# Performance work log

Measured on AMD Instinct MI355X. Metric: run time of the kernel, lower is better.

## Reference

```python
import jax, jax.numpy as jnp
import numpy as np

NBINS = 256       # kornia equalize_clahe default histogram bins
GRID = (8, 8)     # kornia default grid_size


def _clahe(x, clip_limit):
    """kornia-style CLAHE on x:(C,H,W) in [0,1]; H,W divisible by GRID."""
    C, H, W = x.shape
    GH, GW = GRID
    TH, TW = H // GH, W // GW
    pixels = TH * TW
    # ---- per-tile histograms via flat scatter-add (irregular core) ----
    b_hist = jnp.clip((x * NBINS).astype(jnp.int32), 0, NBINS - 1)  # torch.histc(min=0,max=1) bins
    tiles = b_hist.reshape(C, GH, TH, GW, TW).transpose(0, 1, 3, 2, 4).reshape(-1, pixels)
    ntiles = tiles.shape[0]  # C*GH*GW
    flat = (tiles + (jnp.arange(ntiles, dtype=jnp.int32) * NBINS)[:, None]).ravel()
    hist = jnp.zeros((ntiles * NBINS,), x.dtype).at[flat].add(1.0).reshape(ntiles, NBINS)
    # ---- clip and redistribute excess (kornia _compute_luts) ----
    max_val = jnp.maximum(jnp.floor(clip_limit * pixels / NBINS), 1.0)
    clipped = jnp.minimum(hist, max_val)
    excess = pixels - clipped.sum(-1)                    # (ntiles,), >= 0
    residual = jnp.mod(excess, NBINS)
    redist = (excess - residual) / NBINS
    hist = clipped + redist[:, None] + (jnp.arange(NBINS) < residual[:, None]).astype(x.dtype)
    # ---- LUT from CDF ----
    lut = jnp.floor(jnp.clip(jnp.cumsum(hist, -1) * (NBINS - 1) / pixels, 0, NBINS - 1))
    lut = lut.reshape(C, GH, GW, NBINS)
    # ---- per-pixel bilinear interpolation between 4 neighbouring tile LUTs ----
    def coords(n, T, G):
        g = (jnp.arange(n) + 0.5) / T - 0.5    # fractional tile coordinate
        lo = jnp.clip(jnp.floor(g), 0, G - 1).astype(jnp.int32)
        hi = jnp.clip(lo + 1, 0, G - 1)
        w = jnp.clip(g - jnp.floor(g), 0.0, 1.0).astype(x.dtype)
        return lo, hi, w
    y0, y1, wy = coords(H, TH, GH)
    x0, x1, wx = coords(W, TW, GW)
    b = jnp.clip(jnp.floor(x * (NBINS - 1)).astype(jnp.int32), 0, NBINS - 1)  # lookup bin
    c = jnp.arange(C)[:, None, None]
    def g(ty, tx):  # gather lut[c, ty[h], tx[w], b[c,h,w]] -> (C,H,W)
        return lut[c, ty[None, :, None], tx[None, None, :], b]
    top = g(y0, x0) * (1 - wx)[None, None, :] + g(y0, x1) * wx[None, None, :]
    bot = g(y1, x0) * (1 - wx)[None, None, :] + g(y1, x1) * wx[None, None, :]
    out = top * (1 - wy)[None, :, None] + bot * wy[None, :, None]
    return out / (NBINS - 1)


def _forward(x, log_cor=True):
    shape = x.shape
    mean = x.mean()
    std = jnp.std(x, ddof=1)            # torch .std() is unbiased
    x = (x - mean) / std                # TF.normalize
    xmin, xmax = x.min(), x.max()
    x = (x - xmin) / (xmax - xmin)      # normalize_in_range(x, 0, 1)
    ct_proxy = jnp.std(x, ddof=1)       # x.std([0,1,2]) on 3D input = scalar
    def clahe_branch(xx):
        beta = 10.0 * ct_proxy
        cl = 1.0 / (1.0 - beta) + beta  # data-dependent clip limit
        return _clahe(xx, cl)
    x = jax.lax.cond(ct_proxy < 0.05, clahe_branch, lambda xx: xx, x)
    if log_cor:
        x = jnp.log2(1.0 + x)           # adjust_log with gain=1
    return x.reshape(shape)


def setup_inputs() -> dict:
    key = jax.random.key(0)
    x = jax.random.normal(key, (32, 1024, 1024), dtype=jnp.float32)
    # heavy-tailed distribution -> std/range (ct_proxy) ~ 0.01 < 0.05 so CLAHE branch runs
    x = x ** 3
    return {"x": x}


def reference(x):
    return _forward(x, log_cor=True)
```

## Files before the change

### kernel.cpp

```cpp
#include <hip/hip_runtime.h>
#include <math.h>

#define NC 32
#define NH 1024
#define NW 1024
#define NTH 128
#define NTW 128
#define NBINS 256
#define NTILES (NC*8*8)
#define NPIXTOT (NC*NH*NW)
#define TPIX (NTH*NTW)

#define OFF_PSUM   0
#define OFF_PSQ    16384
#define OFF_PMIN   32768
#define OFF_PMAX   40960
#define OFF_PARAMS 49152
#define OFF_LUT8   65536

__global__ __launch_bounds__(256) void k_reduce(const float* __restrict__ x,
                                                double* __restrict__ ps,
                                                double* __restrict__ ps2,
                                                float* __restrict__ pmn,
                                                float* __restrict__ pmx) {
    int tid = threadIdx.x;
    long g = (long)blockIdx.x * 256 + tid;
    double s = 0.0, s2 = 0.0;
    float mn = INFINITY, mx = -INFINITY;
    const float4* x4 = (const float4*)x;
    const long n4 = NPIXTOT / 4;
    for (long i = g; i < n4; i += (long)2048 * 256) {
        float4 v = x4[i];
        float sf  = (v.x + v.y) + (v.z + v.w);
        float s2f = fmaf(v.x, v.x, fmaf(v.y, v.y, fmaf(v.z, v.z, v.w * v.w)));
        s  += (double)sf;
        s2 += (double)s2f;
        mn = fminf(mn, fminf(fminf(v.x, v.y), fminf(v.z, v.w)));
        mx = fmaxf(mx, fmaxf(fmaxf(v.x, v.y), fmaxf(v.z, v.w)));
    }
    for (int o = 32; o; o >>= 1) {
        s  += __shfl_down(s, o);
        s2 += __shfl_down(s2, o);
        mn = fminf(mn, __shfl_down(mn, o));
        mx = fmaxf(mx, __shfl_down(mx, o));
    }
    __shared__ double shs[4], shs2[4];
    __shared__ float shmn[4], shmx[4];
    int wid = tid >> 6, lane = tid & 63;
    if (lane == 0) { shs[wid] = s; shs2[wid] = s2; shmn[wid] = mn; shmx[wid] = mx; }
    __syncthreads();
    if (tid == 0) {
        double S  = shs[0] + shs[1] + shs[2] + shs[3];
        double S2 = shs2[0] + shs2[1] + shs2[2] + shs2[3];
        float MN = fminf(fminf(shmn[0], shmn[1]), fminf(shmn[2], shmn[3]));
        float MX = fmaxf(fmaxf(shmx[0], shmx[1]), fmaxf(shmx[2], shmx[3]));
        ps[blockIdx.x] = S; ps2[blockIdx.x] = S2; pmn[blockIdx.x] = MN; pmx[blockIdx.x] = MX;
    }
}

__global__ __launch_bounds__(256) void k_params(const double* __restrict__ ps,
                                                const double* __restrict__ ps2,
                                                const float* __restrict__ pmn,
                                                const float* __restrict__ pmx,
                                                float* __restrict__ params) {
    int tid = threadIdx.x;
    double s = 0.0, s2 = 0.0;
    float mn = INFINITY, mx = -INFINITY;
    for (int i = tid; i < 2048; i += 256) {
        s += ps[i]; s2 += ps2[i];
        mn = fminf(mn, pmn[i]); mx = fmaxf(mx, pmx[i]);
    }
    for (int o = 32; o; o >>= 1) {
        s  += __shfl_down(s, o);
        s2 += __shfl_down(s2, o);
        mn = fminf(mn, __shfl_down(mn, o));
        mx = fmaxf(mx, __shfl_down(mx, o));
    }
    __shared__ double shs[4], shs2[4];
    __shared__ float shmn[4], shmx[4];
    int wid = tid >> 6, lane = tid & 63;
    if (lane == 0) { shs[wid] = s; shs2[wid] = s2; shmn[wid] = mn; shmx[wid] = mx; }
    __syncthreads();
    if (tid == 0) {
        double S  = shs[0] + shs[1] + shs[2] + shs[3];
        double S2 = shs2[0] + shs2[1] + shs2[2] + shs2[3];
        float MN = fminf(fminf(shmn[0], shmn[1]), fminf(shmn[2], shmn[3]));
        float MX = fmaxf(fmaxf(shmx[0], shmx[1]), fmaxf(shmx[2], shmx[3]));
        const double n = (double)NPIXTOT;
        double var = (S2 - S * S / n) / (n - 1.0);
        double sd = sqrt(var > 0.0 ? var : 0.0);
        double range = (double)MX - (double)MN;
        double ct = sd / range;
        int flag = (ct < 0.05) ? 1 : 0;
        double beta = 10.0 * ct;
        double cl = 1.0 / (1.0 - beta) + beta;
        double mv = floor(cl * (double)TPIX / (double)NBINS);
        if (mv < 1.0) mv = 1.0;
        params[0] = MN;
        params[1] = (float)(1.0 / range);
        params[2] = (float)mv;
        ((int*)params)[3] = flag;
    }
}

__global__ __launch_bounds__(256) void k_histlut(const float* __restrict__ x,
                                                 const float* __restrict__ params,
                                                 unsigned char* __restrict__ lut8) {
    __shared__ unsigned lh[4 * NBINS];
    __shared__ int sh[NBINS];
    int tid = threadIdx.x;
    int t = blockIdx.x;
    int lane = tid & 63;
    int wid = tid >> 6;
    #pragma unroll
    for (int w = 0; w < 4; w++) lh[w * NBINS + tid] = 0;
    __syncthreads();
    float xmin = params[0], inv = params[1];
    int c = t >> 6, gy = (t >> 3) & 7, gx = t & 7;
    const float* base = x + ((long)c * NH + (long)gy * NTH) * NW + gx * NTW;
    unsigned* mylh = lh + wid * NBINS;
    #pragma unroll 4
    for (int j = 0; j < 16; j++) {
        int l = j * 256 + tid;
        int th = l >> 5, tw4 = l & 31;
        float4 v = *(const float4*)(base + (long)th * NW + tw4 * 4);
        float zv[4] = {v.x, v.y, v.z, v.w};
        #pragma unroll
        for (int k = 0; k < 4; k++) {
            float z = (zv[k] - xmin) * inv;
            int b = (int)(z * 256.0f);
            b = b < 0 ? 0 : (b > 255 ? 255 : b);
            unsigned long long alive = __ballot(1);
            #pragma unroll
            for (int r = 0; r < 3; r++) {
                if (!alive) break;
                int leader = (int)(__ffsll((long long)alive) - 1);
                int lb = __shfl(b, leader);
                unsigned long long m = __ballot(b == lb) & alive;
                if (lane == leader) atomicAdd(&mylh[lb], (unsigned)__popcll(m));
                alive &= ~m;
            }
            if ((alive >> lane) & 1ull) atomicAdd(&mylh[b], 1u);
        }
    }
    __syncthreads();
    int mv = (int)params[2];
    int h = (int)(lh[tid] + lh[NBINS + tid] + lh[2 * NBINS + tid] + lh[3 * NBINS + tid]);
    int cl = h < mv ? h : mv;
    sh[tid] = cl;
    __syncthreads();
    for (int o = 1; o < NBINS; o <<= 1) {
        int v = (tid >= o) ? sh[tid - o] : 0;
        __syncthreads();
        sh[tid] += v;
        __syncthreads();
    }
    int total = sh[NBINS - 1];
    int cdfc = sh[tid];
    int excess = TPIX - total;
    int residual = excess & (NBINS - 1);
    int redist = excess >> 8;
    int cdf = cdfc + redist * (tid + 1) + ((tid + 1) < residual ? (tid + 1) : residual);
    float lv = floorf(fminf((float)cdf * 255.0f / 16384.0f, 255.0f));
    int iv = (int)(lv < 0.0f ? 0.0f : lv);
    lut8[t * NBINS + tid] = (unsigned char)iv;
}

__global__ __launch_bounds__(256) void k_out(const float* __restrict__ x,
                                             const float* __restrict__ params,
                                             const unsigned char* __restrict__ lut8,
                                             float* __restrict__ out) {
    __shared__ unsigned char slut[4096];
    int tid = threadIdx.x;
    int r = blockIdx.x;
    int c = r >> 10;
    int h = r & (NH - 1);
    float xmin = params[0], inv = params[1];
    int flag = ((const int*)params)[3];
    float gy = (h + 0.5f) * (1.0f / NTH) - 0.5f;
    float fy = floorf(gy);
    float wy = gy - fy;
    int y0 = (int)fy; y0 = y0 < 0 ? 0 : (y0 > 7 ? 7 : y0);
    int y1 = y0 + 1 > 7 ? 7 : y0 + 1;
    const unsigned char* src0 = lut8 + ((long)c * 64 + y0 * 8) * NBINS;
    const unsigned char* src1 = lut8 + ((long)c * 64 + y1 * 8) * NBINS;
    if (tid < 128) {
        *(uint4*)(slut + tid * 16) = *(const uint4*)(src0 + tid * 16);
    } else {
        int u = tid - 128;
        *(uint4*)(slut + 2048 + u * 16) = *(const uint4*)(src1 + u * 16);
    }
    __syncthreads();
    long p = ((long)r << 10) + tid * 4;
    float4 v = *(const float4*)(x + p);
    float zv[4] = {v.x, v.y, v.z, v.w};
    float o4[4];
    #pragma unroll
    for (int k = 0; k < 4; k++) {
        float z = (zv[k] - xmin) * inv;
        float val;
        if (flag) {
            int wk = tid * 4 + k;
            float gxc = (wk + 0.5f) * (1.0f / NTW) - 0.5f;
            float fx = floorf(gxc);
            float wx = gxc - fx;
            int x0 = (int)fx; x0 = x0 < 0 ? 0 : (x0 > 7 ? 7 : x0);
            int x1 = x0 + 1 > 7 ? 7 : x0 + 1;
            int b = (int)(z * 255.0f);
            b = b < 0 ? 0 : (b > 255 ? 255 : b);
            float l00 = (float)slut[x0 * NBINS + b];
            float l01 = (float)slut[x1 * NBINS + b];
            float l10 = (float)slut[2048 + x0 * NBINS + b];
            float l11 = (float)slut[2048 + x1 * NBINS + b];
            float top = l00 * (1.0f - wx) + l01 * wx;
            float bot = l10 * (1.0f - wx) + l11 * wx;
            val = (top * (1.0f - wy) + bot * wy) * (1.0f / 255.0f);
        } else {
            val = z;
        }
        o4[k] = log2f(1.0f + val);
    }
    *(float4*)(out + p) = make_float4(o4[0], o4[1], o4[2], o4[3]);
}

extern "C" void kernel_launch(void* const* d_in, const int* in_sizes, int n_in,
                              void* d_out, int out_size, void* d_ws, size_t ws_size,
                              hipStream_t stream) {
    const float* x = (const float*)d_in[0];
    float* out = (float*)d_out;
    char* ws = (char*)d_ws;
    double* ps   = (double*)(ws + OFF_PSUM);
    double* ps2  = (double*)(ws + OFF_PSQ);
    float* pmn   = (float*)(ws + OFF_PMIN);
    float* pmx   = (float*)(ws + OFF_PMAX);
    float* params= (float*)(ws + OFF_PARAMS);
    unsigned char* lut8 = (unsigned char*)(ws + OFF_LUT8);

    k_reduce<<<2048, 256, 0, stream>>>(x, ps, ps2, pmn, pmx);
    k_params<<<1, 256, 0, stream>>>(ps, ps2, pmn, pmx, params);
    k_histlut<<<NTILES, 256, 0, stream>>>(x, params, lut8);
    k_out<<<NC * NH, 256, 0, stream>>>(x, params, lut8, out);
}
```

Baseline: 297.8 us.

## Fuse param reduction into histogram kernel and simplify wave-aggregated binning

Removes the single-block k_params launch: every histogram block now redundantly reduces the 2048 partials itself, and block 0 writes params for the output kernel. The histogram inner loop replaces the ballot/leader peeling loop with a single wave-uniform dominant bin taken from lane 0's first pixel. All four pixels per lane are compared against it and counted with one xor-shuffle reduction, and non-matching pixels fall back to per-pixel LDS atomics. The reduction kernel also unrolls by two with split double accumulators to add memory-level parallelism. The trade-off is 2048 redundant partial reads per block, and the histogram speedup depends on the data concentrating in one bin.

```diff
diff --git a/kernel.cpp b/kernel.cpp
--- a/kernel.cpp
+++ b/kernel.cpp
@@ -25,19 +25,31 @@
                                                 float* __restrict__ pmx) {
     int tid = threadIdx.x;
     long g = (long)blockIdx.x * 256 + tid;
-    double s = 0.0, s2 = 0.0;
+    double sa = 0.0, sb = 0.0, s2a = 0.0, s2b = 0.0;
     float mn = INFINITY, mx = -INFINITY;
     const float4* x4 = (const float4*)x;
     const long n4 = NPIXTOT / 4;
-    for (long i = g; i < n4; i += (long)2048 * 256) {
+    const long stride = (long)2048 * 256;
+    for (long i = g; i < n4; i += 2 * stride) {
         float4 v = x4[i];
         float sf  = (v.x + v.y) + (v.z + v.w);
         float s2f = fmaf(v.x, v.x, fmaf(v.y, v.y, fmaf(v.z, v.z, v.w * v.w)));
-        s  += (double)sf;
-        s2 += (double)s2f;
+        sa  += (double)sf;
+        s2a += (double)s2f;
         mn = fminf(mn, fminf(fminf(v.x, v.y), fminf(v.z, v.w)));
         mx = fmaxf(mx, fmaxf(fmaxf(v.x, v.y), fmaxf(v.z, v.w)));
-    }
+        long i2 = i + stride;
+        if (i2 < n4) {
+            float4 u = x4[i2];
+            float sg  = (u.x + u.y) + (u.z + u.w);
+            float s2g = fmaf(u.x, u.x, fmaf(u.y, u.y, fmaf(u.z, u.z, u.w * u.w)));
+            sb  += (double)sg;
+            s2b += (double)s2g;
+            mn = fminf(mn, fminf(fminf(u.x, u.y), fminf(u.z, u.w)));
+            mx = fmaxf(mx, fmaxf(fmaxf(u.x, u.y), fmaxf(u.z, u.w)));
+        }
+    }
+    double s = sa + sb, s2 = s2a + s2b;
     for (int o = 32; o; o >>= 1) {
         s  += __shfl_down(s, o);
         s2 += __shfl_down(s2, o);
@@ -58,12 +70,22 @@
     }
 }
 
-__global__ __launch_bounds__(256) void k_params(const double* __restrict__ ps,
-                                                const double* __restrict__ ps2,
-                                                const float* __restrict__ pmn,
-                                                const float* __restrict__ pmx,
-                                                float* __restrict__ params) {
+__global__ __launch_bounds__(256) void k_histlut(const float* __restrict__ x,
+                                                 const double* __restrict__ ps,
+                                                 const double* __restrict__ ps2,
+                                                 const float* __restrict__ pmn,
+                                                 const float* __restrict__ pmx,
+                                                 float* __restrict__ params,
+                                                 unsigned char* __restrict__ lut8) {
+    __shared__ unsigned lh[4 * NBINS];
+    __shared__ int sh[NBINS];
+    __shared__ double shs[4], shs2[4];
+    __shared__ float shmn[4], shmx[4], spar[4];
     int tid = threadIdx.x;
+    int t = blockIdx.x;
+    int lane = tid & 63;
+    int wid = tid >> 6;
+
     double s = 0.0, s2 = 0.0;
     float mn = INFINITY, mx = -INFINITY;
     for (int i = tid; i < 2048; i += 256) {
@@ -76,9 +98,6 @@
         mn = fminf(mn, __shfl_down(mn, o));
         mx = fmaxf(mx, __shfl_down(mx, o));
     }
-    __shared__ double shs[4], shs2[4];
-    __shared__ float shmn[4], shmx[4];
-    int wid = tid >> 6, lane = tid & 63;
     if (lane == 0) { shs[wid] = s; shs2[wid] = s2; shmn[wid] = mn; shmx[wid] = mx; }
     __syncthreads();
     if (tid == 0) {
@@ -96,26 +115,22 @@
         double cl = 1.0 / (1.0 - beta) + beta;
         double mv = floor(cl * (double)TPIX / (double)NBINS);
         if (mv < 1.0) mv = 1.0;
-        params[0] = MN;
-        params[1] = (float)(1.0 / range);
-        params[2] = (float)mv;
-        ((int*)params)[3] = flag;
-    }
-}
-
-__global__ __launch_bounds__(256) void k_histlut(const float* __restrict__ x,
-                                                 const float* __restrict__ params,
-                                                 unsigned char* __restrict__ lut8) {
-    __shared__ unsigned lh[4 * NBINS];
-    __shared__ int sh[NBINS];
-    int tid = threadIdx.x;
-    int t = blockIdx.x;
-    int lane = tid & 63;
-    int wid = tid >> 6;
+        spar[0] = MN;
+        spar[1] = (float)(1.0 / range);
+        spar[2] = (float)mv;
+        if (t == 0) {
+            params[0] = MN;
+            params[1] = (float)(1.0 / range);
+            params[2] = (float)mv;
+            ((int*)params)[3] = flag;
+        }
+    }
     #pragma unroll
     for (int w = 0; w < 4; w++) lh[w * NBINS + tid] = 0;
     __syncthreads();
-    float xmin = params[0], inv = params[1];
+    float xmin = spar[0], inv = spar[1];
+    int mv = (int)spar[2];
+
     int c = t >> 6, gy = (t >> 3) & 7, gx = t & 7;
     const float* base = x + ((long)c * NH + (long)gy * NTH) * NW + gx * NTW;
     unsigned* mylh = lh + wid * NBINS;
@@ -124,27 +139,26 @@
         int l = j * 256 + tid;
         int th = l >> 5, tw4 = l & 31;
         float4 v = *(const float4*)(base + (long)th * NW + tw4 * 4);
-        float zv[4] = {v.x, v.y, v.z, v.w};
+        float z0 = (v.x - xmin) * inv;
+        float z1 = (v.y - xmin) * inv;
+        float z2 = (v.z - xmin) * inv;
+        float z3 = (v.w - xmin) * inv;
+        int b0 = (int)(z0 * 256.0f); b0 = b0 < 0 ? 0 : (b0 > 255 ? 255 : b0);
+        int b1 = (int)(z1 * 256.0f); b1 = b1 < 0 ? 0 : (b1 > 255 ? 255 : b1);
+        int b2 = (int)(z2 * 256.0f); b2 = b2 < 0 ? 0 : (b2 > 255 ? 255 : b2);
+        int b3 = (int)(z3 * 256.0f); b3 = b3 < 0 ? 0 : (b3 > 255 ? 255 : b3);
+        int d = __builtin_amdgcn_readfirstlane(b0);
+        int cnt = (b0 == d) + (b1 == d) + (b2 == d) + (b3 == d);
         #pragma unroll
-        for (int k = 0; k < 4; k++) {
-            float z = (zv[k] - xmin) * inv;
-            int b = (int)(z * 256.0f);
-            b = b < 0 ? 0 : (b > 255 ? 255 : b);
-            unsigned long long alive = __ballot(1);
-            #pragma unroll
-            for (int r = 0; r < 3; r++) {
-                if (!alive) break;
-                int leader = (int)(__ffsll((long long)alive) - 1);
-                int lb = __shfl(b, leader);
-                unsigned long long m = __ballot(b == lb) & alive;
-                if (lane == leader) atomicAdd(&mylh[lb], (unsigned)__popcll(m));
-                alive &= ~m;
-            }
-            if ((alive >> lane) & 1ull) atomicAdd(&mylh[b], 1u);
-        }
-    }
-    __syncthreads();
-    int mv = (int)params[2];
+        for (int m = 1; m < 64; m <<= 1) cnt += __shfl_xor(cnt, m);
+        if (lane == 0 && cnt > 0) atomicAdd(&mylh[d], (unsigned)cnt);
+        if (b0 != d) atomicAdd(&mylh[b0], 1u);
+        if (b1 != d) atomicAdd(&mylh[b1], 1u);
+        if (b2 != d) atomicAdd(&mylh[b2], 1u);
+        if (b3 != d) atomicAdd(&mylh[b3], 1u);
+    }
+    __syncthreads();
+
     int h = (int)(lh[tid] + lh[NBINS + tid] + lh[2 * NBINS + tid] + lh[3 * NBINS + tid]);
     int cl = h < mv ? h : mv;
     sh[tid] = cl;
@@ -237,7 +251,6 @@
     unsigned char* lut8 = (unsigned char*)(ws + OFF_LUT8);
 
     k_reduce<<<2048, 256, 0, stream>>>(x, ps, ps2, pmn, pmx);
-    k_params<<<1, 256, 0, stream>>>(ps, ps2, pmn, pmx, params);
-    k_histlut<<<NTILES, 256, 0, stream>>>(x, params, lut8);
+    k_histlut<<<NTILES, 256, 0, stream>>>(x, ps, ps2, pmn, pmx, params, lut8);
     k_out<<<NC * NH, 256, 0, stream>>>(x, params, lut8, out);
 }
```

Result: slower. 304.1 us (+2.1%).
